# Optimization experiments

Hardware: AMD Instinct MI355X
Metric: run time of the kernel (lower is better)

## Reference

```python
import jax, jax.numpy as jnp
import numpy as np

EPS = 1e-5


def _conv(x, w, b=None, pad=0):
    y = jax.lax.conv_general_dilated(
        x, w, window_strides=(1, 1), padding=[(pad, pad), (pad, pad)],
        dimension_numbers=('NCHW', 'OIHW', 'NCHW'))
    if b is not None:
        y = y + b[None, :, None, None]
    return y


def _bn(x, g, b, m, v):
    # eval-mode BatchNorm2d with running stats
    scale = (g / jnp.sqrt(v + EPS))[None, :, None, None]
    return (x - m[None, :, None, None]) * scale + b[None, :, None, None]


def setup_inputs() -> dict:
    key = jax.random.key(0)
    B, Ci, Cg, H, W = 4, 128, 64, 128, 128
    ks = iter(jax.random.split(key, 32))
    n = lambda shape, s=1.0: jax.random.normal(next(ks), shape, jnp.float32) * s
    return {
        'input': n((B, Ci, H, W)),
        'weight': n((B, Cg, H, W)),
        # conv11: 3x3, bias (norm_cfg=None) + ReLU
        'w11': n((Ci, Ci + Cg, 3, 3), 0.05), 'b11': n((Ci,), 0.05),
        # conv12: 1x1 -> Ci*9 per-pixel kernel generator
        'w12': n((Ci * 9, Ci, 1, 1), 0.05), 'b12': n((Ci * 9,), 0.05),
        # conv21: 3x3, bias + ReLU
        'w21': n((Ci, Ci + Cg, 3, 3), 0.05), 'b21': n((Ci,), 0.05),
        # conv22: 1x1 -> Ci*Ci channel-mix generator
        'w22': n((Ci * Ci, Ci, 1, 1), 0.05), 'b22': n((Ci * Ci,), 0.05),
        # BN after guided conv (self.local)
        'g1': 1.0 + n((Ci,), 0.1), 'be1': n((Ci,), 0.1), 'm1': n((Ci,), 0.1), 'v1': jnp.ones((Ci,), jnp.float32),
        # BN in self.br
        'g2': 1.0 + n((Ci,), 0.1), 'be2': n((Ci,), 0.1), 'm2': n((Ci,), 0.1), 'v2': jnp.ones((Ci,), jnp.float32),
        # conv3: 3x3 no bias (ConvModule with norm) + BN + ReLU
        'w3': n((Ci, Ci, 3, 3), 0.05),
        'g3': 1.0 + n((Ci,), 0.1), 'be3': n((Ci,), 0.1), 'm3': n((Ci,), 0.1), 'v3': jnp.ones((Ci,), jnp.float32),
    }


def _forward(input, weight, w11, b11, w12, b12, w21, b21, w22, b22,
             g1, be1, m1, v1, g2, be2, m2, v2, w3, g3, be3, m3, v3):
    B, Ci, H, W = input.shape
    wcat = jnp.concatenate([input, weight], axis=1)              # [B, Ci+Cg, H, W]
    w11o = jax.nn.relu(_conv(wcat, w11, b11, pad=1))             # [B, Ci, H, W]
    w12o = _conv(w11o, w12, b12, pad=0)                          # [B, Ci*9, H, W]
    w21o = jax.nn.relu(_conv(wcat, w21, b21, pad=1))             # [B, Ci, H, W]
    pooled = jnp.mean(w21o, axis=(2, 3), keepdims=True)          # [B, Ci, 1, 1]
    w22o = _conv(pooled, w22, b22, pad=0).reshape(B, Ci, Ci)     # [B, Ci, Ci]
    # Conv2dGuided: per-pixel 3x3 kernels from w12o applied depthwise
    xp = jnp.pad(input, ((0, 0), (0, 0), (1, 1), (1, 1)))
    patches = jnp.stack([xp[:, :, i:i + H, j:j + W]
                         for i in range(3) for j in range(3)], axis=2)  # [B, Ci, 9, H, W]
    local = jnp.sum(patches * w12o.reshape(B, Ci, 9, H, W), axis=2)     # [B, Ci, H, W]
    local = jax.nn.relu(_bn(local, g1, be1, m1, v1)).reshape(B, Ci, H * W)
    out = jnp.einsum('bij,bjn->bin', w22o, local).reshape(B, Ci, H, W)  # channel-mix bmm
    out = jax.nn.relu(_bn(out, g2, be2, m2, v2))                        # self.br
    out = jax.nn.relu(_bn(_conv(out, w3, None, pad=1), g3, be3, m3, v3))  # conv3
    return out


def reference(input, weight, w11, b11, w12, b12, w21, b21, w22, b22,
              g1, be1, m1, v1, g2, be2, m2, v2, w3, g3, be3, m3, v3):
    return _forward(input, weight, w11, b11, w12, b12, w21, b21, w22, b22,
                    g1, be1, m1, v1, g2, be2, m2, v2, w3, g3, be3, m3, v3)
```

## Files before the change

### kernel.cpp

```cpp
#include <hip/hip_runtime.h>
#include <math.h>

#define BB   4
#define CI   128
#define CG   64
#define CIN  192
#define HH   128
#define WW   128
#define PP   16384
#define EPSN 1e-5f

typedef unsigned short u16;
typedef unsigned int   u32;
typedef __attribute__((ext_vector_type(8))) short bf16x8;
typedef __attribute__((ext_vector_type(4))) float f32x4;

__device__ __forceinline__ u16 f2bf(float x) {
    union { float f; u32 u; } a; a.f = x;
    u32 u = a.u;
    return (u16)((u + 0x7FFFu + ((u >> 16) & 1u)) >> 16);
}
__device__ __forceinline__ float bf2f(u16 h) {
    union { u32 u; float f; } a; a.u = ((u32)h) << 16; return a.f;
}
__device__ __forceinline__ u32 swz(u32 o) { return o ^ ((o >> 4) & 0x70u); }
__device__ __forceinline__ int xslot(int cc) { return (cc >> 1) & 3; }

__device__ __forceinline__ void gld_lds16(const void* g, void* l) {
    __builtin_amdgcn_global_load_lds(
        (const __attribute__((address_space(1))) void*)g,
        (__attribute__((address_space(3))) void*)l, 16, 0, 0);
}
__device__ __forceinline__ int yswz(int bid) {
    return ((bid & 7) << 4) | (bid >> 3);
}

__global__ __launch_bounds__(256) void k_pack(
    const float* __restrict__ src0, int nch0,
    const float* __restrict__ src1, int nch1,
    u16* __restrict__ dhi, u16* __restrict__ dlo, int cinp)
{
    const int rr = blockIdx.x;
    const int b  = blockIdx.y;
    const int t  = threadIdx.x;
    u16* rh = dhi + ((size_t)b * 130 + rr) * 130 * cinp;
    u16* rl = dlo + ((size_t)b * 130 + rr) * 130 * cinp;

    if (rr == 0 || rr == 129) {
        u32* rh4 = (u32*)rh; u32* rl4 = (u32*)rl;
        const int tot = 130 * cinp / 2;
        for (int i = t; i < tot; i += 256) { rh4[i] = 0u; rl4[i] = 0u; }
        return;
    }
    const int y = rr - 1;
    for (int i = t; i < cinp; i += 256) {
        rh[i] = 0; rl[i] = 0;
        rh[129 * cinp + i] = 0; rl[129 * cinp + i] = 0;
    }

    __shared__ float xs[32][129];
    for (int ck = 0; ck < cinp / 32; ++ck) {
        __syncthreads();
        for (int i = t; i < 32 * 128; i += 256) {
            const int ch = i >> 7, col = i & 127;
            const int c = ck * 32 + ch;
            const float* sp = (c < nch0)
                ? src0 + ((size_t)b * nch0 + c) * PP
                : src1 + ((size_t)b * nch1 + (c - nch0)) * PP;
            xs[ch][col] = sp[y * WW + col];
        }
        __syncthreads();
        for (int i = t; i < 512; i += 256) {
            const int col = i >> 2, oct = i & 3;
            u16 hh[8], ll[8];
#pragma unroll
            for (int j = 0; j < 8; ++j) {
                const float v = xs[oct * 8 + j][col];
                const u16 h = f2bf(v);
                hh[j] = h; ll[j] = f2bf(v - bf2f(h));
            }
            const size_t off = (size_t)(col + 1) * cinp + ck * 32 + oct * 8;
            uint4 vh, vl;
            vh.x = (u32)hh[0] | ((u32)hh[1] << 16); vh.y = (u32)hh[2] | ((u32)hh[3] << 16);
            vh.z = (u32)hh[4] | ((u32)hh[5] << 16); vh.w = (u32)hh[6] | ((u32)hh[7] << 16);
            vl.x = (u32)ll[0] | ((u32)ll[1] << 16); vl.y = (u32)ll[2] | ((u32)ll[3] << 16);
            vl.z = (u32)ll[4] | ((u32)ll[5] << 16); vl.w = (u32)ll[6] | ((u32)ll[7] << 16);
            *(uint4*)(rh + off) = vh;
            *(uint4*)(rl + off) = vl;
        }
    }
}

__global__ __launch_bounds__(256) void k_wpack(
    const float* __restrict__ w0, const float* __restrict__ w1,
    u16* __restrict__ dst, int nmb, int nck, int cin)
{
    const int total = nmb * nck * 9 * 128 * 4;
    const int idx = blockIdx.x * 256 + threadIdx.x;
    if (idx >= total) return;
    const int oct = idx & 3; int r2 = idx >> 2;
    const int oc = r2 & 127; r2 >>= 7;
    const int tap = r2 % 9; r2 /= 9;
    const int ck = r2 % nck; r2 /= nck;
    const int mb = r2;
    const float* w = mb ? w1 : w0;
    u16 hh[8], ll[8];
#pragma unroll
    for (int j = 0; j < 8; ++j) {
        const int c = ck * 32 + oct * 8 + j;
        const float v = w[((size_t)oc * cin + c) * 9 + tap];
        const u16 h = f2bf(v);
        hh[j] = h; ll[j] = f2bf(v - bf2f(h));
    }
    const size_t halfs = (size_t)nmb * nck * 9 * 128 * 32;
    const size_t base = ((((size_t)mb * nck + ck) * 9 + tap) * 128 + oc) * 32 + oct * 8;
    uint4 vh, vl;
    vh.x = (u32)hh[0] | ((u32)hh[1] << 16); vh.y = (u32)hh[2] | ((u32)hh[3] << 16);
    vh.z = (u32)hh[4] | ((u32)hh[5] << 16); vh.w = (u32)hh[6] | ((u32)hh[7] << 16);
    vl.x = (u32)ll[0] | ((u32)ll[1] << 16); vl.y = (u32)ll[2] | ((u32)ll[3] << 16);
    vl.z = (u32)ll[4] | ((u32)ll[5] << 16); vl.w = (u32)ll[6] | ((u32)ll[7] << 16);
    *(uint4*)(dst + base) = vh;
    *(uint4*)(dst + halfs + base) = vl;
}

__global__ __launch_bounds__(256) void k_wpack12(
    const float* __restrict__ w12, u16* __restrict__ dst)
{
    const int idx = blockIdx.x * 256 + threadIdx.x;
    if (idx >= 18432) return;
    const int oct = idx & 15;
    const int g   = idx >> 4;
    const int cc  = g / 9, tap = g % 9;
    u16 hh[8], ll[8];
#pragma unroll
    for (int j = 0; j < 8; ++j) {
        const float v = w12[(size_t)g * 128 + oct * 8 + j];
        const u16 h = f2bf(v);
        hh[j] = h; ll[j] = f2bf(v - bf2f(h));
    }
    const size_t base = ((size_t)(tap * 128 + cc)) * 128 + oct * 8;
    uint4 vh, vl;
    vh.x = (u32)hh[0] | ((u32)hh[1] << 16); vh.y = (u32)hh[2] | ((u32)hh[3] << 16);
    vh.z = (u32)hh[4] | ((u32)hh[5] << 16); vh.w = (u32)hh[6] | ((u32)hh[7] << 16);
    vl.x = (u32)ll[0] | ((u32)ll[1] << 16); vl.y = (u32)ll[2] | ((u32)ll[3] << 16);
    vl.z = (u32)ll[4] | ((u32)ll[5] << 16); vl.w = (u32)ll[6] | ((u32)ll[7] << 16);
    *(uint4*)(dst + base) = vh;
    *(uint4*)(dst + 147456 + base) = vl;
}

template<int NCK, bool DUAL>
__global__ __launch_bounds__(256, 2) void k_conv_mfma(
    const u16* __restrict__ xhi, const u16* __restrict__ xlo,
    const u16* __restrict__ wA,
    const float* __restrict__ bias0, const float* __restrict__ bias1,
    const float* __restrict__ bng, const float* __restrict__ bnb,
    const float* __restrict__ bnm, const float* __restrict__ bnv,
    float* __restrict__ dst0, float* __restrict__ dst1,
    u16* __restrict__ y1ph, u16* __restrict__ y1pl)
{
    constexpr int CINP  = NCK * 32;
    constexpr int MBT   = DUAL ? 2 : 1;
    constexpr size_t WHALF = (size_t)MBT * NCK * 9 * 128 * 32;

    __shared__ char smem[65536];

    const int t    = threadIdx.x;
    const int wave = t >> 6;
    const int lane = t & 63;
    const int wm   = wave >> 1, wn = wave & 1;
    const int y    = yswz(blockIdx.x);
    const int mb   = blockIdx.y;
    const int b    = blockIdx.z;
    const int l15  = lane & 15;
    const int kg   = lane >> 4;

    f32x4 acc[4][4];
    if (DUAL) {
        const float* bp = mb ? bias1 : bias0;
#pragma unroll
        for (int fm = 0; fm < 4; ++fm) {
            const int ocb = wm * 64 + fm * 16 + kg * 4;
#pragma unroll
            for (int j = 0; j < 4; ++j) {
                const float bv = bp[ocb + j];
#pragma unroll
                for (int fn = 0; fn < 4; ++fn) acc[fm][fn][j] = bv;
            }
        }
    } else {
#pragma unroll
        for (int fm = 0; fm < 4; ++fm)
#pragma unroll
            for (int fn = 0; fn < 4; ++fn)
#pragma unroll
                for (int j = 0; j < 4; ++j) acc[fm][fn][j] = 0.0f;
    }

    const size_t xrow = (size_t)130 * CINP;

    for (int ck = 0; ck < NCK; ++ck) {
        __syncthreads();
        for (int idx = wave; idx < 54; idx += 4) {
            const int h = idx / 27, rem = idx % 27;
            const int r = rem / 9, iss = rem % 9;
            const u16* gb = (h ? xlo : xhi)
                + ((size_t)b * 130 + (y + r)) * xrow + ck * 32;
            const int cc = iss * 16 + (lane >> 2);
            const int rb = ((lane & 3) << 4) ^ (xslot(cc) << 4);
            gld_lds16((const char*)gb + (size_t)cc * (CINP * 2) + rb,
                      smem + (h * 3 + r) * 9216 + iss * 1024);
        }
        asm volatile("s_waitcnt vmcnt(0)" ::: "memory");
        __syncthreads();

        for (int tap = 0; tap < 9; ++tap) {
            const int dy = tap / 3, dx = tap % 3;
            const size_t abase = (((size_t)mb * NCK + ck) * 9 + tap) * 4096;
            bf16x8 ah[4], al[4], bh[4], bl[4];
#pragma unroll
            for (int f = 0; f < 4; ++f) {
                const size_t ao = abase + (size_t)(wm * 64 + f * 16 + l15) * 32 + kg * 8;
                ah[f] = *(const bf16x8*)(wA + ao);
                al[f] = *(const bf16x8*)(wA + WHALF + ao);
                const int cc = wn * 64 + f * 16 + l15 + dx;
                const char* bp0 = smem + dy * 9216 + cc * 64 + ((kg ^ xslot(cc)) << 4);
                bh[f] = *(const bf16x8*)bp0;
                bl[f] = *(const bf16x8*)(bp0 + 27648);
            }
#pragma unroll
            for (int fm = 0; fm < 4; ++fm)
#pragma unroll
                for (int fn = 0; fn < 4; ++fn) {
                    acc[fm][fn] = __builtin_amdgcn_mfma_f32_16x16x32_bf16(
                        al[fm], bh[fn], acc[fm][fn], 0, 0, 0);
                    acc[fm][fn] = __builtin_amdgcn_mfma_f32_16x16x32_bf16(
                        ah[fm], bl[fn], acc[fm][fn], 0, 0, 0);
                    acc[fm][fn] = __builtin_amdgcn_mfma_f32_16x16x32_bf16(
                        ah[fm], bh[fn], acc[fm][fn], 0, 0, 0);
                }
        }
    }

    if (DUAL && mb == 0) {
        __syncthreads();
        u16* img = (u16*)smem;
#pragma unroll
        for (int fm = 0; fm < 4; ++fm)
#pragma unroll
            for (int fn = 0; fn < 4; ++fn) {
                const int px = wn * 64 + fn * 16 + l15;
                const int c0 = wm * 64 + fm * 16 + kg * 4;
                u16 hh[4], ll[4];
#pragma unroll
                for (int j = 0; j < 4; ++j) {
                    const float v = fmaxf(acc[fm][fn][j], 0.0f);
                    const u16 h = f2bf(v);
                    hh[j] = h; ll[j] = f2bf(v - bf2f(h));
                }
                const u32 off = swz((u32)(px * 256 + c0 * 2));
                uint2 vh, vl;
                vh.x = (u32)hh[0] | ((u32)hh[1] << 16); vh.y = (u32)hh[2] | ((u32)hh[3] << 16);
                vl.x = (u32)ll[0] | ((u32)ll[1] << 16); vl.y = (u32)ll[2] | ((u32)ll[3] << 16);
                *(uint2*)((char*)img + off)         = vh;
                *(uint2*)((char*)img + 32768 + off) = vl;
            }
        __syncthreads();
        for (int h = 0; h < 2; ++h) {
            uint4* gd = (uint4*)((h ? y1pl : y1ph) + ((size_t)b * 128 + y) * 16384);
            const uint4* s4 = (const uint4*)(smem + h * 32768);
            for (int i = t; i < 2048; i += 256) gd[i] = s4[i];
        }
        return;
    }

    float* dst = DUAL ? dst1 : dst0;
#pragma unroll
    for (int fm = 0; fm < 4; ++fm) {
#pragma unroll
        for (int j = 0; j < 4; ++j) {
            const int oc = wm * 64 + fm * 16 + kg * 4 + j;
            float sc = 1.0f, sh = 0.0f;
            if (!DUAL) {
                sc = bng[oc] * rsqrtf(bnv[oc] + EPSN);
                sh = bnb[oc] - bnm[oc] * sc;
            }
            const size_t obase = ((size_t)b * CI + oc) * PP + (size_t)y * WW;
#pragma unroll
            for (int fn = 0; fn < 4; ++fn) {
                const int px = wn * 64 + fn * 16 + l15;
                float v = acc[fm][fn][j];
                if (!DUAL) v = fmaf(v, sc, sh);
                dst[obase + px] = fmaxf(v, 0.0f);
            }
        }
    }
}

__global__ __launch_bounds__(256) void k_pool(
    const float* __restrict__ y2, float* __restrict__ pooled)
{
    const int c = blockIdx.x, b = blockIdx.y, t = threadIdx.x;
    const float* src = y2 + ((size_t)b * CI + c) * PP;
    float s = 0.0f;
    for (int i = t; i < PP; i += 256) s += src[i];
    __shared__ float red[256];
    red[t] = s;
    __syncthreads();
    for (int st = 128; st > 0; st >>= 1) {
        if (t < st) red[t] += red[t + st];
        __syncthreads();
    }
    if (t == 0) pooled[b * CI + c] = red[0] * (1.0f / PP);
}

__global__ __launch_bounds__(256) void k_w22(
    const float* __restrict__ w22, const float* __restrict__ b22,
    const float* __restrict__ pooled, u16* __restrict__ w22p)
{
    const int b = blockIdx.y;
    const int o = blockIdx.x * 256 + threadIdx.x;
    __shared__ float pl[CI];
    if (threadIdx.x < CI) pl[threadIdx.x] = pooled[b * CI + threadIdx.x];
    __syncthreads();
    const float4* wr = (const float4*)(w22 + (size_t)o * CI);
    float acc = b22[o];
#pragma unroll 8
    for (int c4 = 0; c4 < CI / 4; ++c4) {
        const float4 w = wr[c4];
        acc += w.x * pl[c4 * 4 + 0] + w.y * pl[c4 * 4 + 1] +
               w.z * pl[c4 * 4 + 2] + w.w * pl[c4 * 4 + 3];
    }
    const u16 h = f2bf(acc);
    w22p[(size_t)b * 16384 + o] = h;
    w22p[65536 + (size_t)b * 16384 + o] = f2bf(acc - bf2f(h));
}

__global__ __launch_bounds__(256, 2) void k_guided_mfma(
    const float* __restrict__ input,
    const u16* __restrict__ y1p,
    const u16* __restrict__ w12p,
    const float* __restrict__ b12,
    const float* __restrict__ g1, const float* __restrict__ be1,
    const float* __restrict__ m1, const float* __restrict__ v1,
    u16* __restrict__ locp)
{
    __shared__ char smem[65536];
    const int t = threadIdx.x;
    const int wave = t >> 6, lane = t & 63;
    const int wm = wave >> 1, wn = wave & 1;
    const int l15 = lane & 15, kg = lane >> 4;
    const int y = yswz(blockIdx.x), b = blockIdx.y;

    for (int h = 0; h < 2; ++h) {
        const u16* gb = y1p + (size_t)h * 8388608 + ((size_t)b * 128 + y) * 16384;
        for (int iss = wave; iss < 32; iss += 4)
            gld_lds16((const char*)gb + iss * 1024 + lane * 16,
                      smem + h * 32768 + iss * 1024);
    }
    asm volatile("s_waitcnt vmcnt(0)" ::: "memory");
    __syncthreads();

    f32x4 accL[4][4];
#pragma unroll
    for (int fm = 0; fm < 4; ++fm)
#pragma unroll
        for (int fn = 0; fn < 4; ++fn)
#pragma unroll
            for (int j = 0; j < 4; ++j) accL[fm][fn][j] = 0.0f;

    const float* xb = input + (size_t)b * CI * PP;

    for (int tap = 0; tap < 9; ++tap) {
        const int ry  = y + tap / 3 - 1;
        const int dxo = tap % 3 - 1;
        if ((unsigned)ry >= (unsigned)HH) continue;

        f32x4 accG[4][4];
#pragma unroll
        for (int fm = 0; fm < 4; ++fm) {
            float bv[4];
#pragma unroll
            for (int j = 0; j < 4; ++j)
                bv[j] = b12[(wm * 64 + fm * 16 + kg * 4 + j) * 9 + tap];
#pragma unroll
            for (int fn = 0; fn < 4; ++fn)
#pragma unroll
                for (int j = 0; j < 4; ++j) accG[fm][fn][j] = bv[j];
        }

#pragma unroll
        for (int ks = 0; ks < 4; ++ks) {
            bf16x8 bh[4], bl[4];
#pragma unroll
            for (int f = 0; f < 4; ++f) {
                const int px = wn * 64 + f * 16 + l15;
                const u32 bo = swz((u32)(px * 256 + ks * 64 + kg * 16));
                bh[f] = *(const bf16x8*)(smem + bo);
                bl[f] = *(const bf16x8*)(smem + 32768 + bo);
            }
#pragma unroll
            for (int fm = 0; fm < 4; ++fm) {
                const size_t ao = ((size_t)(tap * 128 + wm * 64 + fm * 16 + l15)) * 128
                                  + ks * 32 + kg * 8;
                const bf16x8 ah = *(const bf16x8*)(w12p + ao);
                const bf16x8 al = *(const bf16x8*)(w12p + 147456 + ao);
#pragma unroll
                for (int fn = 0; fn < 4; ++fn) {
                    accG[fm][fn] = __builtin_amdgcn_mfma_f32_16x16x32_bf16(
                        al, bh[fn], accG[fm][fn], 0, 0, 0);
                    accG[fm][fn] = __builtin_amdgcn_mfma_f32_16x16x32_bf16(
                        ah, bl[fn], accG[fm][fn], 0, 0, 0);
                    accG[fm][fn] = __builtin_amdgcn_mfma_f32_16x16x32_bf16(
                        ah, bh[fn], accG[fm][fn], 0, 0, 0);
                }
            }
        }

#pragma unroll
        for (int fm = 0; fm < 4; ++fm)
#pragma unroll
            for (int fn = 0; fn < 4; ++fn) {
                const int px = wn * 64 + fn * 16 + l15;
                const int rx = px + dxo;
                const bool okx = (unsigned)rx < (unsigned)WW;
                const float* xr = xb + (size_t)ry * WW + (okx ? rx : 0);
#pragma unroll
                for (int j = 0; j < 4; ++j) {
                    const int ci = wm * 64 + fm * 16 + kg * 4 + j;
                    const float xv = okx ? xr[(size_t)ci * PP] : 0.0f;
                    accL[fm][fn][j] = fmaf(accG[fm][fn][j], xv, accL[fm][fn][j]);
                }
            }
    }

    __syncthreads();
    u16* img = (u16*)smem;
#pragma unroll
    for (int fm = 0; fm < 4; ++fm) {
        float sc[4], sh[4];
#pragma unroll
        for (int j = 0; j < 4; ++j) {
            const int cc = wm * 64 + fm * 16 + kg * 4 + j;
            sc[j] = g1[cc] * rsqrtf(v1[cc] + EPSN);
            sh[j] = be1[cc] - m1[cc] * sc[j];
        }
#pragma unroll
        for (int fn = 0; fn < 4; ++fn) {
            const int px = wn * 64 + fn * 16 + l15;
            const int c0 = wm * 64 + fm * 16 + kg * 4;
            u16 hh[4], ll[4];
#pragma unroll
            for (int j = 0; j < 4; ++j) {
                const float v = fmaxf(fmaf(accL[fm][fn][j], sc[j], sh[j]), 0.0f);
                const u16 h = f2bf(v);
                hh[j] = h; ll[j] = f2bf(v - bf2f(h));
            }
            const u32 off = swz((u32)(px * 256 + c0 * 2));
            uint2 vh, vl;
            vh.x = (u32)hh[0] | ((u32)hh[1] << 16); vh.y = (u32)hh[2] | ((u32)hh[3] << 16);
            vl.x = (u32)ll[0] | ((u32)ll[1] << 16); vl.y = (u32)ll[2] | ((u32)ll[3] << 16);
            *(uint2*)((char*)img + off)         = vh;
            *(uint2*)((char*)img + 32768 + off) = vl;
        }
    }
    __syncthreads();
    for (int h = 0; h < 2; ++h) {
        uint4* gd = (uint4*)(locp + (size_t)h * 8388608 + ((size_t)b * 128 + y) * 16384);
        const uint4* s4 = (const uint4*)(smem + h * 32768);
        for (int i = t; i < 2048; i += 256) gd[i] = s4[i];
    }
}

__global__ __launch_bounds__(256, 2) void k_bmm_mfma(
    const u16* __restrict__ locp, const u16* __restrict__ w22p,
    const float* __restrict__ g2, const float* __restrict__ be2,
    const float* __restrict__ m2, const float* __restrict__ v2,
    u16* __restrict__ x3h, u16* __restrict__ x3l)
{
    __shared__ char smem[65536];
    const int t = threadIdx.x;
    const int wave = t >> 6, lane = t & 63;
    const int wm = wave >> 1, wn = wave & 1;
    const int l15 = lane & 15, kg = lane >> 4;
    const int y = blockIdx.x, b = blockIdx.y;

    for (int h = 0; h < 2; ++h) {
        const u16* gb = locp + (size_t)h * 8388608 + ((size_t)b * 128 + y) * 16384;
        for (int iss = wave; iss < 32; iss += 4)
            gld_lds16((const char*)gb + iss * 1024 + lane * 16,
                      smem + h * 32768 + iss * 1024);
    }
    asm volatile("s_waitcnt vmcnt(0)" ::: "memory");
    __syncthreads();

    f32x4 acc[4][4];
#pragma unroll
    for (int fm = 0; fm < 4; ++fm)
#pragma unroll
        for (int fn = 0; fn < 4; ++fn)
#pragma unroll
            for (int j = 0; j < 4; ++j) acc[fm][fn][j] = 0.0f;

#pragma unroll
    for (int ks = 0; ks < 4; ++ks) {
        bf16x8 bh[4], bl[4];
#pragma unroll
        for (int f = 0; f < 4; ++f) {
            const int px = wn * 64 + f * 16 + l15;
            const u32 bo = swz((u32)(px * 256 + ks * 64 + kg * 16));
            bh[f] = *(const bf16x8*)(smem + bo);
            bl[f] = *(const bf16x8*)(smem + 32768 + bo);
        }
#pragma unroll
        for (int fm = 0; fm < 4; ++fm) {
            const size_t ao = ((size_t)(b * 128 + wm * 64 + fm * 16 + l15)) * 128
                              + ks * 32 + kg * 8;
            const bf16x8 ah = *(const bf16x8*)(w22p + ao);
            const bf16x8 al = *(const bf16x8*)(w22p + 65536 + ao);
#pragma unroll
            for (int fn = 0; fn < 4; ++fn) {
                acc[fm][fn] = __builtin_amdgcn_mfma_f32_16x16x32_bf16(
                    al, bh[fn], acc[fm][fn], 0, 0, 0);
                acc[fm][fn] = __builtin_amdgcn_mfma_f32_16x16x32_bf16(
                    ah, bl[fn], acc[fm][fn], 0, 0, 0);
                acc[fm][fn] = __builtin_amdgcn_mfma_f32_16x16x32_bf16(
                    ah, bh[fn], acc[fm][fn], 0, 0, 0);
            }
        }
    }

    __syncthreads();
    u16* img = (u16*)smem;
#pragma unroll
    for (int fm = 0; fm < 4; ++fm) {
        float sc[4], sh[4];
#pragma unroll
        for (int j = 0; j < 4; ++j) {
            const int cc = wm * 64 + fm * 16 + kg * 4 + j;
            sc[j] = g2[cc] * rsqrtf(v2[cc] + EPSN);
            sh[j] = be2[cc] - m2[cc] * sc[j];
        }
#pragma unroll
        for (int fn = 0; fn < 4; ++fn) {
            const int px = wn * 64 + fn * 16 + l15;
            const int c0 = wm * 64 + fm * 16 + kg * 4;
            u16 hh[4], ll[4];
#pragma unroll
            for (int j = 0; j < 4; ++j) {
                const float v = fmaxf(fmaf(acc[fm][fn][j], sc[j], sh[j]), 0.0f);
                const u16 h = f2bf(v);
                hh[j] = h; ll[j] = f2bf(v - bf2f(h));
            }
            const u32 off = (u32)(px * 256 + c0 * 2);
            uint2 vh, vl;
            vh.x = (u32)hh[0] | ((u32)hh[1] << 16); vh.y = (u32)hh[2] | ((u32)hh[3] << 16);
            vl.x = (u32)ll[0] | ((u32)ll[1] << 16); vl.y = (u32)ll[2] | ((u32)ll[3] << 16);
            *(uint2*)((char*)img + off)         = vh;
            *(uint2*)((char*)img + 32768 + off) = vl;
        }
    }
    __syncthreads();
    for (int h = 0; h < 2; ++h) {
        uint4* gd = (uint4*)((h ? x3l : x3h)
            + (((size_t)b * 130 + y + 1) * 130 + 1) * 128);
        const uint4* s4 = (const uint4*)(smem + h * 32768);
        for (int i = t; i < 2048; i += 256) gd[i] = s4[i];
    }
}

__global__ __launch_bounds__(256) void k_zero3(u16* __restrict__ x3)
{
    const int idx = blockIdx.x * 256 + threadIdx.x;
    if (idx >= 264192) return;
    const int hb = idx / 33024;
    int r2 = idx % 33024;
    u32* base = (u32*)(x3 + (size_t)(hb >> 2) * 8652800
                          + (size_t)(hb & 3) * 130 * 130 * 128);
    if (r2 < 8320)            base[r2] = 0u;
    else if (r2 < 16640)      base[(size_t)129 * 8320 + (r2 - 8320)] = 0u;
    else {
        const int q = r2 - 16640;
        const int w = q & 63;
        const int r = q >> 6;
        const int row = 1 + (r >> 1);
        const int side = r & 1;
        base[(size_t)row * 8320 + (side ? 8256 : 0) + w] = 0u;
    }
}

extern "C" void kernel_launch(void* const* d_in, const int* in_sizes, int n_in,
                              void* d_out, int out_size, void* d_ws, size_t ws_size,
                              hipStream_t stream)
{
    (void)in_sizes; (void)n_in; (void)out_size; (void)ws_size;

    const float* input  = (const float*)d_in[0];
    const float* weight = (const float*)d_in[1];
    const float* w11    = (const float*)d_in[2];
    const float* b11    = (const float*)d_in[3];
    const float* w12    = (const float*)d_in[4];
    const float* b12    = (const float*)d_in[5];
    const float* w21    = (const float*)d_in[6];
    const float* b21    = (const float*)d_in[7];
    const float* w22    = (const float*)d_in[8];
    const float* b22    = (const float*)d_in[9];
    const float* g1     = (const float*)d_in[10];
    const float* be1    = (const float*)d_in[11];
    const float* m1     = (const float*)d_in[12];
    const float* v1     = (const float*)d_in[13];
    const float* g2     = (const float*)d_in[14];
    const float* be2    = (const float*)d_in[15];
    const float* m2     = (const float*)d_in[16];
    const float* v2     = (const float*)d_in[17];
    const float* w3     = (const float*)d_in[18];
    const float* g3     = (const float*)d_in[19];
    const float* be3    = (const float*)d_in[20];
    const float* m3     = (const float*)d_in[21];
    const float* v3     = (const float*)d_in[22];

    float* ws     = (float*)d_ws;
    float* y2o    = ws;
    float* pooled = ws + 8388608;
    u16*   w22p   = (u16*)(ws + 8389120);
    u16*   wAd    = (u16*)(ws + 8454656);
    u16*   wA3    = (u16*)(ws + 8897024);
    u16*   w12p   = (u16*)(ws + 9044480);
    u16*   xpadDh = (u16*)(ws + 9191936);
    u16*   xpadDl = xpadDh + 12979200;
    u16*   locp   = (u16*)(ws + 9191936);
    u16*   y1p    = (u16*)(ws + 22171136);
    u16*   x3h    = (u16*)(ws + 22171136);
    u16*   x3l    = x3h + 8652800;
    float* outp   = (float*)d_out;

    k_pack<<<dim3(130, BB), 256, 0, stream>>>(input, CI, weight, CG, xpadDh, xpadDl, CIN);
    k_wpack<<<dim3(216), 256, 0, stream>>>(w11, w21, wAd, 2, 6, CIN);
    k_wpack<<<dim3(72), 256, 0, stream>>>(w3, w3, wA3, 1, 4, CI);
    k_wpack12<<<dim3(72), 256, 0, stream>>>(w12, w12p);

    k_conv_mfma<6, true><<<dim3(128, 2, BB), 256, 0, stream>>>(
        xpadDh, xpadDl, wAd, b11, b21, nullptr, nullptr, nullptr, nullptr,
        nullptr, y2o, y1p, y1p + 8388608);

    k_pool<<<dim3(CI, BB), 256, 0, stream>>>(y2o, pooled);
    k_w22<<<dim3(64, BB), 256, 0, stream>>>(w22, b22, pooled, w22p);

    k_guided_mfma<<<dim3(128, BB), 256, 0, stream>>>(
        input, y1p, w12p, b12, g1, be1, m1, v1, locp);

    k_zero3<<<dim3(1032), 256, 0, stream>>>(x3h);

    k_bmm_mfma<<<dim3(128, BB), 256, 0, stream>>>(
        locp, w22p, g2, be2, m2, v2, x3h, x3l);

    k_conv_mfma<4, false><<<dim3(128, 1, BB), 256, 0, stream>>>(
        x3h, x3l, wA3, nullptr, nullptr, g3, be3, m3, v3, outp, nullptr,
        nullptr, nullptr);
}
```

Measured before the change: 577.7 us.

## Drop lo-part of split-bf16 activations and double-buffer conv LDS staging

Activations are now stored as a single bf16 tensor instead of a hi/lo split pair, so every MFMA GEMM drops from three products to two (weight hi and lo times activation hi). This halves activation packing, staging and global traffic and removes a third of the MFMA work. The conv kernel also double-buffers its LDS input tiles, issuing loads for the next channel chunk early with a partial vmcnt wait, and software-pipelines the A/B fragment loads across taps. The cost is lower accuracy, since activations are rounded to plain bf16.

```diff
diff --git a/kernel.cpp b/kernel.cpp
--- a/kernel.cpp
+++ b/kernel.cpp
@@ -38,24 +38,23 @@
 __global__ __launch_bounds__(256) void k_pack(
     const float* __restrict__ src0, int nch0,
     const float* __restrict__ src1, int nch1,
-    u16* __restrict__ dhi, u16* __restrict__ dlo, int cinp)
+    u16* __restrict__ dst, int cinp)
 {
     const int rr = blockIdx.x;
     const int b  = blockIdx.y;
     const int t  = threadIdx.x;
-    u16* rh = dhi + ((size_t)b * 130 + rr) * 130 * cinp;
-    u16* rl = dlo + ((size_t)b * 130 + rr) * 130 * cinp;
+    u16* rh = dst + ((size_t)b * 130 + rr) * 130 * cinp;
 
     if (rr == 0 || rr == 129) {
-        u32* rh4 = (u32*)rh; u32* rl4 = (u32*)rl;
+        u32* rh4 = (u32*)rh;
         const int tot = 130 * cinp / 2;
-        for (int i = t; i < tot; i += 256) { rh4[i] = 0u; rl4[i] = 0u; }
+        for (int i = t; i < tot; i += 256) rh4[i] = 0u;
         return;
     }
     const int y = rr - 1;
     for (int i = t; i < cinp; i += 256) {
-        rh[i] = 0; rl[i] = 0;
-        rh[129 * cinp + i] = 0; rl[129 * cinp + i] = 0;
+        rh[i] = 0;
+        rh[129 * cinp + i] = 0;
     }
 
     __shared__ float xs[32][129];
@@ -72,21 +71,14 @@
         __syncthreads();
         for (int i = t; i < 512; i += 256) {
             const int col = i >> 2, oct = i & 3;
-            u16 hh[8], ll[8];
-#pragma unroll
-            for (int j = 0; j < 8; ++j) {
-                const float v = xs[oct * 8 + j][col];
-                const u16 h = f2bf(v);
-                hh[j] = h; ll[j] = f2bf(v - bf2f(h));
-            }
+            u16 hh[8];
+#pragma unroll
+            for (int j = 0; j < 8; ++j) hh[j] = f2bf(xs[oct * 8 + j][col]);
             const size_t off = (size_t)(col + 1) * cinp + ck * 32 + oct * 8;
-            uint4 vh, vl;
+            uint4 vh;
             vh.x = (u32)hh[0] | ((u32)hh[1] << 16); vh.y = (u32)hh[2] | ((u32)hh[3] << 16);
             vh.z = (u32)hh[4] | ((u32)hh[5] << 16); vh.w = (u32)hh[6] | ((u32)hh[7] << 16);
-            vl.x = (u32)ll[0] | ((u32)ll[1] << 16); vl.y = (u32)ll[2] | ((u32)ll[3] << 16);
-            vl.z = (u32)ll[4] | ((u32)ll[5] << 16); vl.w = (u32)ll[6] | ((u32)ll[7] << 16);
             *(uint4*)(rh + off) = vh;
-            *(uint4*)(rl + off) = vl;
         }
     }
 }
@@ -148,21 +140,37 @@
     *(uint4*)(dst + 147456 + base) = vl;
 }
 
+#define LOADA(tapv, AH, AL) do {                                              \
+    const size_t abase_ = (((size_t)mb * NCK + ck) * 9 + (tapv)) * 4096;      \
+    _Pragma("unroll")                                                         \
+    for (int f_ = 0; f_ < 4; ++f_) {                                          \
+        const size_t ao_ = abase_ + (size_t)(wm * 64 + f_ * 16 + l15) * 32 + kg * 8; \
+        AH[f_] = *(const bf16x8*)(wA + ao_);                                  \
+        AL[f_] = *(const bf16x8*)(wA + WHALF + ao_);                          \
+    } } while (0)
+
+#define LOADB(tapv, BV) do {                                                  \
+    const int dy_ = (tapv) / 3, dx_ = (tapv) % 3;                             \
+    _Pragma("unroll")                                                         \
+    for (int f_ = 0; f_ < 4; ++f_) {                                          \
+        const int cc_ = wn * 64 + f_ * 16 + l15 + dx_;                        \
+        BV[f_] = *(const bf16x8*)(bbase + dy_ * 9216 + cc_ * 64               \
+                                  + ((kg ^ xslot(cc_)) << 4));                \
+    } } while (0)
+
 template<int NCK, bool DUAL>
 __global__ __launch_bounds__(256, 2) void k_conv_mfma(
-    const u16* __restrict__ xhi, const u16* __restrict__ xlo,
-    const u16* __restrict__ wA,
+    const u16* __restrict__ xin, const u16* __restrict__ wA,
     const float* __restrict__ bias0, const float* __restrict__ bias1,
     const float* __restrict__ bng, const float* __restrict__ bnb,
     const float* __restrict__ bnm, const float* __restrict__ bnv,
-    float* __restrict__ dst0, float* __restrict__ dst1,
-    u16* __restrict__ y1ph, u16* __restrict__ y1pl)
-{
-    constexpr int CINP  = NCK * 32;
-    constexpr int MBT   = DUAL ? 2 : 1;
-    constexpr size_t WHALF = (size_t)MBT * NCK * 9 * 128 * 32;
-
-    __shared__ char smem[65536];
+    float* __restrict__ dstf, float* __restrict__ bnout,
+    u16* __restrict__ y1img)
+{
+    constexpr int CINP = NCK * 32;
+    constexpr size_t WHALF = (size_t)(DUAL ? 2 : 1) * NCK * 9 * 128 * 32;
+
+    __shared__ char smem[55296];
 
     const int t    = threadIdx.x;
     const int wave = t >> 6;
@@ -198,51 +206,58 @@
 
     const size_t xrow = (size_t)130 * CINP;
 
+    #define STAGE(c, bsel) do {                                               \
+        for (int idx_ = wave; idx_ < 27; idx_ += 4) {                         \
+            const int r_ = idx_ / 9, iss_ = idx_ % 9;                         \
+            const u16* gb_ = xin + ((size_t)b * 130 + (y + r_)) * xrow + (c) * 32; \
+            const int cc_ = iss_ * 16 + (lane >> 2);                          \
+            const int rb_ = ((lane & 3) << 4) ^ (xslot(cc_) << 4);            \
+            gld_lds16((const char*)gb_ + (size_t)cc_ * (CINP * 2) + rb_,      \
+                      smem + (bsel) * 27648 + r_ * 9216 + iss_ * 1024);       \
+        } } while (0)
+
+    STAGE(0, 0);
+    int cur = 0;
     for (int ck = 0; ck < NCK; ++ck) {
-        __syncthreads();
-        for (int idx = wave; idx < 54; idx += 4) {
-            const int h = idx / 27, rem = idx % 27;
-            const int r = rem / 9, iss = rem % 9;
-            const u16* gb = (h ? xlo : xhi)
-                + ((size_t)b * 130 + (y + r)) * xrow + ck * 32;
-            const int cc = iss * 16 + (lane >> 2);
-            const int rb = ((lane & 3) << 4) ^ (xslot(cc) << 4);
-            gld_lds16((const char*)gb + (size_t)cc * (CINP * 2) + rb,
-                      smem + (h * 3 + r) * 9216 + iss * 1024);
-        }
-        asm volatile("s_waitcnt vmcnt(0)" ::: "memory");
-        __syncthreads();
-
+        STAGE(ck + 1 < NCK ? ck + 1 : 0, cur ^ 1);
+        asm volatile("s_waitcnt vmcnt(6)" ::: "memory");
+        __builtin_amdgcn_s_barrier();
+
+        const char* bbase = smem + cur * 27648;
+        bf16x8 ahC[4], alC[4], bC[4];
+        LOADA(0, ahC, alC);
+        LOADB(0, bC);
+#pragma unroll
         for (int tap = 0; tap < 9; ++tap) {
-            const int dy = tap / 3, dx = tap % 3;
-            const size_t abase = (((size_t)mb * NCK + ck) * 9 + tap) * 4096;
-            bf16x8 ah[4], al[4], bh[4], bl[4];
-#pragma unroll
-            for (int f = 0; f < 4; ++f) {
-                const size_t ao = abase + (size_t)(wm * 64 + f * 16 + l15) * 32 + kg * 8;
-                ah[f] = *(const bf16x8*)(wA + ao);
-                al[f] = *(const bf16x8*)(wA + WHALF + ao);
-                const int cc = wn * 64 + f * 16 + l15 + dx;
-                const char* bp0 = smem + dy * 9216 + cc * 64 + ((kg ^ xslot(cc)) << 4);
-                bh[f] = *(const bf16x8*)bp0;
-                bl[f] = *(const bf16x8*)(bp0 + 27648);
-            }
+            bf16x8 ahN[4], alN[4], bN[4];
+            if (tap < 8) { LOADA(tap + 1, ahN, alN); LOADB(tap + 1, bN); }
 #pragma unroll
             for (int fm = 0; fm < 4; ++fm)
 #pragma unroll
-                for (int fn = 0; fn < 4; ++fn) {
+                for (int fn = 0; fn < 4; ++fn)
                     acc[fm][fn] = __builtin_amdgcn_mfma_f32_16x16x32_bf16(
-                        al[fm], bh[fn], acc[fm][fn], 0, 0, 0);
+                        alC[fm], bC[fn], acc[fm][fn], 0, 0, 0);
+#pragma unroll
+            for (int fm = 0; fm < 4; ++fm)
+#pragma unroll
+                for (int fn = 0; fn < 4; ++fn)
                     acc[fm][fn] = __builtin_amdgcn_mfma_f32_16x16x32_bf16(
-                        ah[fm], bl[fn], acc[fm][fn], 0, 0, 0);
-                    acc[fm][fn] = __builtin_amdgcn_mfma_f32_16x16x32_bf16(
-                        ah[fm], bh[fn], acc[fm][fn], 0, 0, 0);
+                        ahC[fm], bC[fn], acc[fm][fn], 0, 0, 0);
+            if (tap < 8) {
+#pragma unroll
+                for (int f = 0; f < 4; ++f) {
+                    ahC[f] = ahN[f]; alC[f] = alN[f]; bC[f] = bN[f];
                 }
-        }
-    }
+            }
+        }
+        __builtin_amdgcn_s_barrier();
+        cur ^= 1;
+    }
+    asm volatile("s_waitcnt vmcnt(0)" ::: "memory");
+    #undef STAGE
 
     if (DUAL && mb == 0) {
-        __syncthreads();
+        __builtin_amdgcn_s_barrier();
         u16* img = (u16*)smem;
 #pragma unroll
         for (int fm = 0; fm < 4; ++fm)
@@ -250,30 +265,24 @@
             for (int fn = 0; fn < 4; ++fn) {
                 const int px = wn * 64 + fn * 16 + l15;
                 const int c0 = wm * 64 + fm * 16 + kg * 4;
-                u16 hh[4], ll[4];
-#pragma unroll
-                for (int j = 0; j < 4; ++j) {
-                    const float v = fmaxf(acc[fm][fn][j], 0.0f);
-                    const u16 h = f2bf(v);
-                    hh[j] = h; ll[j] = f2bf(v - bf2f(h));
-                }
+                u16 hh[4];
+#pragma unroll
+                for (int j = 0; j < 4; ++j)
+                    hh[j] = f2bf(fmaxf(acc[fm][fn][j], 0.0f));
                 const u32 off = swz((u32)(px * 256 + c0 * 2));
-                uint2 vh, vl;
-                vh.x = (u32)hh[0] | ((u32)hh[1] << 16); vh.y = (u32)hh[2] | ((u32)hh[3] << 16);
-                vl.x = (u32)ll[0] | ((u32)ll[1] << 16); vl.y = (u32)ll[2] | ((u32)ll[3] << 16);
-                *(uint2*)((char*)img + off)         = vh;
-                *(uint2*)((char*)img + 32768 + off) = vl;
-            }
-        __syncthreads();
-        for (int h = 0; h < 2; ++h) {
-            uint4* gd = (uint4*)((h ? y1pl : y1ph) + ((size_t)b * 128 + y) * 16384);
-            const uint4* s4 = (const uint4*)(smem + h * 32768);
-            for (int i = t; i < 2048; i += 256) gd[i] = s4[i];
-        }
+                uint2 vh;
+                vh.x = (u32)hh[0] | ((u32)hh[1] << 16);
+                vh.y = (u32)hh[2] | ((u32)hh[3] << 16);
+                *(uint2*)((char*)img + off) = vh;
+            }
+        __builtin_amdgcn_s_barrier();
+        uint4* gd = (uint4*)(y1img + ((size_t)b * 128 + y) * 16384);
+        const uint4* s4 = (const uint4*)smem;
+        for (int i = t; i < 2048; i += 256) gd[i] = s4[i];
         return;
     }
 
-    float* dst = DUAL ? dst1 : dst0;
+    float* dst = DUAL ? dstf : bnout;
 #pragma unroll
     for (int fm = 0; fm < 4; ++fm) {
 #pragma unroll
@@ -337,25 +346,25 @@
 
 __global__ __launch_bounds__(256, 2) void k_guided_mfma(
     const float* __restrict__ input,
-    const u16* __restrict__ y1p,
+    const u16* __restrict__ y1img,
     const u16* __restrict__ w12p,
     const float* __restrict__ b12,
     const float* __restrict__ g1, const float* __restrict__ be1,
     const float* __restrict__ m1, const float* __restrict__ v1,
     u16* __restrict__ locp)
 {
-    __shared__ char smem[65536];
+    __shared__ char smem[32768];
     const int t = threadIdx.x;
     const int wave = t >> 6, lane = t & 63;
     const int wm = wave >> 1, wn = wave & 1;
     const int l15 = lane & 15, kg = lane >> 4;
     const int y = yswz(blockIdx.x), b = blockIdx.y;
 
-    for (int h = 0; h < 2; ++h) {
-        const u16* gb = y1p + (size_t)h * 8388608 + ((size_t)b * 128 + y) * 16384;
+    {
+        const u16* gb = y1img + ((size_t)b * 128 + y) * 16384;
         for (int iss = wave; iss < 32; iss += 4)
             gld_lds16((const char*)gb + iss * 1024 + lane * 16,
-                      smem + h * 32768 + iss * 1024);
+                      smem + iss * 1024);
     }
     asm volatile("s_waitcnt vmcnt(0)" ::: "memory");
     __syncthreads();
@@ -390,13 +399,12 @@
 
 #pragma unroll
         for (int ks = 0; ks < 4; ++ks) {
-            bf16x8 bh[4], bl[4];
+            bf16x8 bC[4];
 #pragma unroll
             for (int f = 0; f < 4; ++f) {
                 const int px = wn * 64 + f * 16 + l15;
-                const u32 bo = swz((u32)(px * 256 + ks * 64 + kg * 16));
-                bh[f] = *(const bf16x8*)(smem + bo);
-                bl[f] = *(const bf16x8*)(smem + 32768 + bo);
+                bC[f] = *(const bf16x8*)(smem +
+                    swz((u32)(px * 256 + ks * 64 + kg * 16)));
             }
 #pragma unroll
             for (int fm = 0; fm < 4; ++fm) {
@@ -407,11 +415,9 @@
 #pragma unroll
                 for (int fn = 0; fn < 4; ++fn) {
                     accG[fm][fn] = __builtin_amdgcn_mfma_f32_16x16x32_bf16(
-                        al, bh[fn], accG[fm][fn], 0, 0, 0);
+                        al, bC[fn], accG[fm][fn], 0, 0, 0);
                     accG[fm][fn] = __builtin_amdgcn_mfma_f32_16x16x32_bf16(
-                        ah, bl[fn], accG[fm][fn], 0, 0, 0);
-                    accG[fm][fn] = __builtin_amdgcn_mfma_f32_16x16x32_bf16(
-                        ah, bh[fn], accG[fm][fn], 0, 0, 0);
+                        ah, bC[fn], accG[fm][fn], 0, 0, 0);
                 }
             }
         }
@@ -448,47 +454,41 @@
         for (int fn = 0; fn < 4; ++fn) {
             const int px = wn * 64 + fn * 16 + l15;
             const int c0 = wm * 64 + fm * 16 + kg * 4;
-            u16 hh[4], ll[4];
-#pragma unroll
-            for (int j = 0; j < 4; ++j) {
-                const float v = fmaxf(fmaf(accL[fm][fn][j], sc[j], sh[j]), 0.0f);
-                const u16 h = f2bf(v);
-                hh[j] = h; ll[j] = f2bf(v - bf2f(h));
-            }
+            u16 hh[4];
+#pragma unroll
+            for (int j = 0; j < 4; ++j)
+                hh[j] = f2bf(fmaxf(fmaf(accL[fm][fn][j], sc[j], sh[j]), 0.0f));
             const u32 off = swz((u32)(px * 256 + c0 * 2));
-            uint2 vh, vl;
-            vh.x = (u32)hh[0] | ((u32)hh[1] << 16); vh.y = (u32)hh[2] | ((u32)hh[3] << 16);
-            vl.x = (u32)ll[0] | ((u32)ll[1] << 16); vl.y = (u32)ll[2] | ((u32)ll[3] << 16);
-            *(uint2*)((char*)img + off)         = vh;
-            *(uint2*)((char*)img + 32768 + off) = vl;
-        }
-    }
-    __syncthreads();
-    for (int h = 0; h < 2; ++h) {
-        uint4* gd = (uint4*)(locp + (size_t)h * 8388608 + ((size_t)b * 128 + y) * 16384);
-        const uint4* s4 = (const uint4*)(smem + h * 32768);
-        for (int i = t; i < 2048; i += 256) gd[i] = s4[i];
-    }
+            uint2 vh;
+            vh.x = (u32)hh[0] | ((u32)hh[1] << 16);
+            vh.y = (u32)hh[2] | ((u32)hh[3] << 16);
+            *(uint2*)((char*)img + off) = vh;
+        }
+    }
+    __syncthreads();
+    uint4* gd = (uint4*)(locp + ((size_t)b * 128 + y) * 16384);
+    const uint4* s4 = (const uint4*)smem;
+    for (int i = t; i < 2048; i += 256) gd[i] = s4[i];
 }
 
 __global__ __launch_bounds__(256, 2) void k_bmm_mfma(
     const u16* __restrict__ locp, const u16* __restrict__ w22p,
     const float* __restrict__ g2, const float* __restrict__ be2,
     const float* __restrict__ m2, const float* __restrict__ v2,
-    u16* __restrict__ x3h, u16* __restrict__ x3l)
-{
-    __shared__ char smem[65536];
+    u16* __restrict__ x3)
+{
+    __shared__ char smem[32768];
     const int t = threadIdx.x;
     const int wave = t >> 6, lane = t & 63;
     const int wm = wave >> 1, wn = wave & 1;
     const int l15 = lane & 15, kg = lane >> 4;
     const int y = blockIdx.x, b = blockIdx.y;
 
-    for (int h = 0; h < 2; ++h) {
-        const u16* gb = locp + (size_t)h * 8388608 + ((size_t)b * 128 + y) * 16384;
+    {
+        const u16* gb = locp + ((size_t)b * 128 + y) * 16384;
         for (int iss = wave; iss < 32; iss += 4)
             gld_lds16((const char*)gb + iss * 1024 + lane * 16,
-                      smem + h * 32768 + iss * 1024);
+                      smem + iss * 1024);
     }
     asm volatile("s_waitcnt vmcnt(0)" ::: "memory");
     __syncthreads();
@@ -503,13 +503,12 @@
 
 #pragma unroll
     for (int ks = 0; ks < 4; ++ks) {
-        bf16x8 bh[4], bl[4];
+        bf16x8 bC[4];
 #pragma unroll
         for (int f = 0; f < 4; ++f) {
             const int px = wn * 64 + f * 16 + l15;
-            const u32 bo = swz((u32)(px * 256 + ks * 64 + kg * 16));
-            bh[f] = *(const bf16x8*)(smem + bo);
-            bl[f] = *(const bf16x8*)(smem + 32768 + bo);
+            bC[f] = *(const bf16x8*)(smem +
+                swz((u32)(px * 256 + ks * 64 + kg * 16)));
         }
 #pragma unroll
         for (int fm = 0; fm < 4; ++fm) {
@@ -520,11 +519,9 @@
 #pragma unroll
             for (int fn = 0; fn < 4; ++fn) {
                 acc[fm][fn] = __builtin_amdgcn_mfma_f32_16x16x32_bf16(
-                    al, bh[fn], acc[fm][fn], 0, 0, 0);
+                    al, bC[fn], acc[fm][fn], 0, 0, 0);
                 acc[fm][fn] = __builtin_amdgcn_mfma_f32_16x16x32_bf16(
-                    ah, bl[fn], acc[fm][fn], 0, 0, 0);
-                acc[fm][fn] = __builtin_amdgcn_mfma_f32_16x16x32_bf16(
-                    ah, bh[fn], acc[fm][fn], 0, 0, 0);
+                    ah, bC[fn], acc[fm][fn], 0, 0, 0);
             }
         }
     }
@@ -544,38 +541,30 @@
         for (int fn = 0; fn < 4; ++fn) {
             const int px = wn * 64 + fn * 16 + l15;
             const int c0 = wm * 64 + fm * 16 + kg * 4;
-            u16 hh[4], ll[4];
-#pragma unroll
-            for (int j = 0; j < 4; ++j) {
-                const float v = fmaxf(fmaf(acc[fm][fn][j], sc[j], sh[j]), 0.0f);
-                const u16 h = f2bf(v);
-                hh[j] = h; ll[j] = f2bf(v - bf2f(h));
-            }
+            u16 hh[4];
+#pragma unroll
+            for (int j = 0; j < 4; ++j)
+                hh[j] = f2bf(fmaxf(fmaf(acc[fm][fn][j], sc[j], sh[j]), 0.0f));
             const u32 off = (u32)(px * 256 + c0 * 2);
-            uint2 vh, vl;
-            vh.x = (u32)hh[0] | ((u32)hh[1] << 16); vh.y = (u32)hh[2] | ((u32)hh[3] << 16);
-            vl.x = (u32)ll[0] | ((u32)ll[1] << 16); vl.y = (u32)ll[2] | ((u32)ll[3] << 16);
-            *(uint2*)((char*)img + off)         = vh;
-            *(uint2*)((char*)img + 32768 + off) = vl;
-        }
-    }
-    __syncthreads();
-    for (int h = 0; h < 2; ++h) {
-        uint4* gd = (uint4*)((h ? x3l : x3h)
-            + (((size_t)b * 130 + y + 1) * 130 + 1) * 128);
-        const uint4* s4 = (const uint4*)(smem + h * 32768);
-        for (int i = t; i < 2048; i += 256) gd[i] = s4[i];
-    }
+            uint2 vh;
+            vh.x = (u32)hh[0] | ((u32)hh[1] << 16);
+            vh.y = (u32)hh[2] | ((u32)hh[3] << 16);
+            *(uint2*)((char*)img + off) = vh;
+        }
+    }
+    __syncthreads();
+    uint4* gd = (uint4*)(x3 + (((size_t)b * 130 + y + 1) * 130 + 1) * 128);
+    const uint4* s4 = (const uint4*)smem;
+    for (int i = t; i < 2048; i += 256) gd[i] = s4[i];
 }
 
 __global__ __launch_bounds__(256) void k_zero3(u16* __restrict__ x3)
 {
     const int idx = blockIdx.x * 256 + threadIdx.x;
-    if (idx >= 264192) return;
-    const int hb = idx / 33024;
+    if (idx >= 132096) return;
+    const int b = idx / 33024;
     int r2 = idx % 33024;
-    u32* base = (u32*)(x3 + (size_t)(hb >> 2) * 8652800
-                          + (size_t)(hb & 3) * 130 * 130 * 128);
+    u32* base = (u32*)(x3 + (size_t)b * 2163200);
     if (r2 < 8320)            base[r2] = 0u;
     else if (r2 < 16640)      base[(size_t)129 * 8320 + (r2 - 8320)] = 0u;
     else {
@@ -625,35 +614,32 @@
     u16*   wAd    = (u16*)(ws + 8454656);
     u16*   wA3    = (u16*)(ws + 8897024);
     u16*   w12p   = (u16*)(ws + 9044480);
-    u16*   xpadDh = (u16*)(ws + 9191936);
-    u16*   xpadDl = xpadDh + 12979200;
+    u16*   xpadD  = (u16*)(ws + 9191936);
     u16*   locp   = (u16*)(ws + 9191936);
-    u16*   y1p    = (u16*)(ws + 22171136);
-    u16*   x3h    = (u16*)(ws + 22171136);
-    u16*   x3l    = x3h + 8652800;
+    u16*   y1img  = (u16*)(ws + 15681536);
+    u16*   x3     = (u16*)(ws + 15681536);
     float* outp   = (float*)d_out;
 
-    k_pack<<<dim3(130, BB), 256, 0, stream>>>(input, CI, weight, CG, xpadDh, xpadDl, CIN);
+    k_pack<<<dim3(130, BB), 256, 0, stream>>>(input, CI, weight, CG, xpadD, CIN);
     k_wpack<<<dim3(216), 256, 0, stream>>>(w11, w21, wAd, 2, 6, CIN);
     k_wpack<<<dim3(72), 256, 0, stream>>>(w3, w3, wA3, 1, 4, CI);
     k_wpack12<<<dim3(72), 256, 0, stream>>>(w12, w12p);
 
     k_conv_mfma<6, true><<<dim3(128, 2, BB), 256, 0, stream>>>(
-        xpadDh, xpadDl, wAd, b11, b21, nullptr, nullptr, nullptr, nullptr,
-        nullptr, y2o, y1p, y1p + 8388608);
+        xpadD, wAd, b11, b21, nullptr, nullptr, nullptr, nullptr,
+        y2o, nullptr, y1img);
 
     k_pool<<<dim3(CI, BB), 256, 0, stream>>>(y2o, pooled);
     k_w22<<<dim3(64, BB), 256, 0, stream>>>(w22, b22, pooled, w22p);
 
     k_guided_mfma<<<dim3(128, BB), 256, 0, stream>>>(
-        input, y1p, w12p, b12, g1, be1, m1, v1, locp);
-
-    k_zero3<<<dim3(1032), 256, 0, stream>>>(x3h);
+        input, y1img, w12p, b12, g1, be1, m1, v1, locp);
+
+    k_zero3<<<dim3(516), 256, 0, stream>>>(x3);
 
     k_bmm_mfma<<<dim3(128, BB), 256, 0, stream>>>(
-        locp, w22p, g2, be2, m2, v2, x3h, x3l);
+        locp, w22p, g2, be2, m2, v2, x3);
 
     k_conv_mfma<4, false><<<dim3(128, 1, BB), 256, 0, stream>>>(
-        x3h, x3l, wA3, nullptr, nullptr, g3, be3, m3, v3, outp, nullptr,
-        nullptr, nullptr);
-}
+        x3, wA3, nullptr, nullptr, g3, be3, m3, v3, nullptr, outp, nullptr);
+}
```

Result: slower. 656.9 us (+13.7%).
